# Kernel optimization log

Measured on AMD Instinct MI355X. Metric: run time of the kernel, lower is better.

Reference implementation:

```python
import jax, jax.numpy as jnp
import numpy as np

BATCH = 64
N_NODES = 1000
SEQ = 12
FEAT = 4          # in_features_per_node // N_history
IN_CH = 48        # in_features_per_node, also GAT out_channels
HEADS = 2
OUT_FEAT = 2      # out_features_per_node
H1, H2 = 256, 128
N_TOTAL = BATCH * N_NODES
E = 1024000


def setup_inputs() -> dict:
    key = jax.random.key(0)
    ks = jax.random.split(key, 16)
    s = 0.05
    return {
        "x": jax.random.normal(ks[0], (N_TOTAL, IN_CH), jnp.float32),
        "edge_index": jax.random.randint(ks[1], (2, E), 0, N_TOTAL, jnp.int64),
        "W_gat": jax.random.normal(ks[2], (IN_CH, HEADS * IN_CH), jnp.float32) * s,
        "att_src": jax.random.normal(ks[3], (HEADS, IN_CH), jnp.float32) * s,
        "att_dst": jax.random.normal(ks[4], (HEADS, IN_CH), jnp.float32) * s,
        "gat_bias": jax.random.normal(ks[5], (IN_CH,), jnp.float32) * s,
        "W_ih1": jax.random.normal(ks[6], (4 * H1, N_NODES * FEAT), jnp.float32) * s,
        "W_hh1": jax.random.normal(ks[7], (4 * H1, H1), jnp.float32) * s,
        "b1": jnp.zeros((4 * H1,), jnp.float32),
        "W_ih2": jax.random.normal(ks[8], (4 * H2, H1), jnp.float32) * s,
        "W_hh2": jax.random.normal(ks[9], (4 * H2, H2), jnp.float32) * s,
        "b2": jnp.zeros((4 * H2,), jnp.float32),
        "W_out": jax.random.normal(ks[10], (N_NODES * OUT_FEAT, H2), jnp.float32) * s,
        "b_out": jnp.zeros((N_NODES * OUT_FEAT,), jnp.float32),
    }


def _gat_conv(x, edge_index, W_gat, att_src, att_dst, gat_bias):
    """PyG GATConv, heads=HEADS, concat=False (mean over heads), add_self_loops=True."""
    N = x.shape[0]
    h = (x @ W_gat).reshape(N, HEADS, IN_CH)              # [N,H,C]
    a_src = jnp.einsum('nhc,hc->nh', h, att_src)          # [N,H]
    a_dst = jnp.einsum('nhc,hc->nh', h, att_dst)
    loops = jnp.arange(N, dtype=edge_index.dtype)
    src = jnp.concatenate([edge_index[0], loops])         # [E+N]
    dst = jnp.concatenate([edge_index[1], loops])
    e = jax.nn.leaky_relu(a_src[src] + a_dst[dst], 0.2)   # [E+N,H]
    # segment-softmax over incoming edges of each destination node
    m = jnp.full((N, HEADS), -jnp.inf, e.dtype).at[dst].max(e)
    w = jnp.exp(e - m[dst])
    denom = jax.ops.segment_sum(w, dst, num_segments=N)
    alpha = w / (denom[dst] + 1e-16)                      # [E+N,H]
    msg = h[src] * alpha[:, :, None]                      # [E+N,H,C]
    out = jax.ops.segment_sum(msg, dst, num_segments=N)   # [N,H,C]
    return out.mean(axis=1) + gat_bias                    # [N,C]


def _lstm(x_seq, W_ih, W_hh, b):
    """Single-layer LSTM, PyTorch gate order (i,f,g,o). x_seq: [T,B,D]."""
    Hs = W_hh.shape[1]
    B = x_seq.shape[1]
    xw = jnp.einsum('tbd,gd->tbg', x_seq, W_ih) + b       # precompute input proj

    def step(carry, xt):
        h, c = carry
        g = xt + h @ W_hh.T
        i, f, gg, o = jnp.split(g, 4, axis=-1)
        i, f, o = jax.nn.sigmoid(i), jax.nn.sigmoid(f), jax.nn.sigmoid(o)
        c = f * c + i * jnp.tanh(gg)
        h = o * jnp.tanh(c)
        return (h, c), h

    h0 = jnp.zeros((B, Hs), x_seq.dtype)
    _, ys = jax.lax.scan(step, (h0, h0), xw)
    return ys                                             # [T,B,Hs]


def reference(x, edge_index, W_gat, att_src, att_dst, gat_bias,
              W_ih1, W_hh1, b1, W_ih2, W_hh2, b2, W_out, b_out):
    g = _gat_conv(x, edge_index, W_gat, att_src, att_dst, gat_bias)  # [N_total, 48]
    # (B, N_nodes, SEQ, FEAT) -> movedim(2,0) -> (SEQ, B, N_nodes*FEAT)
    g = g.reshape(BATCH, N_NODES, SEQ, FEAT)
    g = jnp.moveaxis(g, 2, 0).reshape(SEQ, BATCH, N_NODES * FEAT)
    y = _lstm(g, W_ih1, W_hh1, b1)
    y = _lstm(y, W_ih2, W_hh2, b2)
    last = y[-1]                                          # [B, H2]
    out = last @ W_out.T + b_out                          # [B, N_nodes*OUT_FEAT]
    return out.reshape(BATCH * N_NODES, OUT_FEAT)
```

## Files before the change

### kernel.cpp

```cpp
#include <hip/hip_runtime.h>
#include <hip/hip_fp16.h>
#include <math.h>

#define NTOT   64000
#define NNODE  1000
#define NBATCH 64
#define NSEQ   12
#define NE     1024000

typedef _Float16 half8 __attribute__((ext_vector_type(8)));
typedef float f32x4 __attribute__((ext_vector_type(4)));

__device__ __forceinline__ float lrelu(float x){ return x > 0.f ? x : 0.2f*x; }
__device__ __forceinline__ float sigmoidf_(float x){ return 1.f/(1.f+__expf(-x)); }

__global__ void __launch_bounds__(256) k_gat_count(const float* __restrict__ x, const float* __restrict__ Wg,
                       const float* __restrict__ att_s, const float* __restrict__ att_d,
                       __half* __restrict__ hfeat, float* __restrict__ asrc, float* __restrict__ adst,
                       const int* __restrict__ ei, int* __restrict__ cnt){
  if (blockIdx.x >= 250){
    int e = (blockIdx.x - 250)*256 + threadIdx.x;
    if (e < NE) atomicAdd(&cnt[ei[NE + e]], 1);
    return;
  }
  __shared__ __align__(16) float Ws[48*96];
  __shared__ float as_s[96], ad_s[96];
  for (int i = threadIdx.x; i < 48*96; i += 256) Ws[i] = Wg[i];
  if (threadIdx.x < 96){ as_s[threadIdx.x] = att_s[threadIdx.x]; ad_s[threadIdx.x] = att_d[threadIdx.x]; }
  __syncthreads();
  int n = blockIdx.x * 256 + threadIdx.x;
  float xr[48];
  const float4* xv = (const float4*)(x + (size_t)n*48);
  #pragma unroll
  for (int q = 0; q < 12; ++q){ float4 v = xv[q]; xr[q*4]=v.x; xr[q*4+1]=v.y; xr[q*4+2]=v.z; xr[q*4+3]=v.w; }
  float a0=0.f,a1=0.f,d0=0.f,d1=0.f;
  __half* hrow = hfeat + (size_t)n*96;
  float prev = 0.f;
  for (int j = 0; j < 96; ++j){
    float acc = 0.f;
    #pragma unroll
    for (int k = 0; k < 48; ++k) acc += xr[k]*Ws[k*96+j];
    if (j & 1){
      __half2 p; p.x = __float2half(prev); p.y = __float2half(acc);
      *(__half2*)(hrow + j - 1) = p;
    } else prev = acc;
    if (j < 48){ a0 += acc*as_s[j]; d0 += acc*ad_s[j]; }
    else       { a1 += acc*as_s[j]; d1 += acc*ad_s[j]; }
  }
  asrc[n*2]=a0; asrc[n*2+1]=a1; adst[n*2]=d0; adst[n*2+1]=d1;
}

__global__ void __launch_bounds__(256) k_scan1(const int* __restrict__ cnt, int* __restrict__ wsum){
  int w = (blockIdx.x*256 + threadIdx.x) >> 6;
  int lane = threadIdx.x & 63;
  int v = cnt[w*64 + lane];
  int t = v;
  #pragma unroll
  for (int d = 1; d < 64; d <<= 1) t += __shfl_xor(t, d);
  if (lane == 0) wsum[w] = t;
}

__global__ void __launch_bounds__(1024) k_scan2(int* __restrict__ wsum){
  __shared__ int tmp[1024];
  int k = threadIdx.x;
  int v = (k < 1000) ? wsum[k] : 0;
  tmp[k] = v; __syncthreads();
  for (int d = 1; d < 1024; d <<= 1){
    int t = (k >= d) ? tmp[k-d] : 0;
    __syncthreads();
    tmp[k] += t;
    __syncthreads();
  }
  if (k < 1000) wsum[k] = tmp[k] - v;
}

__global__ void __launch_bounds__(256) k_scan3(const int* __restrict__ cnt, const int* __restrict__ wpre,
                                               int* __restrict__ offs, int* __restrict__ cursor){
  int w = (blockIdx.x*256 + threadIdx.x) >> 6;
  int lane = threadIdx.x & 63;
  int i = w*64 + lane;
  int v = cnt[i];
  int x = v;
  #pragma unroll
  for (int d = 1; d < 64; d <<= 1){
    int t = __shfl_up(x, d);
    if (lane >= d) x += t;
  }
  int excl = wpre[w] + x - v;
  offs[i] = excl; cursor[i] = excl;
  if (i == NTOT-1) offs[NTOT] = excl + v;
}

__global__ void k_scatter(const int* __restrict__ ei, int* __restrict__ cursor, int* __restrict__ csr){
  int e = blockIdx.x*256 + threadIdx.x;
  if (e < NE){
    int d = ei[NE + e], s = ei[e];
    int pos = atomicAdd(&cursor[d], 1);
    csr[pos] = s;
  }
}

__global__ void __launch_bounds__(256) k_node(const __half* __restrict__ hf, const float* __restrict__ asrc,
                      const float* __restrict__ adst, const int* __restrict__ offs,
                      const int* __restrict__ csr, const float* __restrict__ bias,
                      _Float16* __restrict__ xseqh){
  __shared__ float gsh[4][96];
  int wv = threadIdx.x >> 6, lane = threadIdx.x & 63;
  int n = blockIdx.x*4 + wv;
  int off = offs[n], deg = offs[n+1] - off;
  const float2* as2 = (const float2*)asrc;
  float2 adn = ((const float2*)adst)[n];
  float2 asn = as2[n];
  float es0 = __expf(lrelu(asn.x + adn.x));
  float es1 = __expf(lrelu(asn.y + adn.y));
  if (lane < 48){
    int cl = lane;
    bool h0 = (lane < 24);
    float wself = h0 ? es0 : es1;
    float ssum = wself;
    float2 acc;
    {
      __half2 r2 = *(const __half2*)(hf + (size_t)n*96 + 2*cl);
      float2 r = __half22float2(r2);
      acc.x = r.x*wself; acc.y = r.y*wself;
    }
    int i = 0;
    for (; i + 4 <= deg; i += 4){
      int ss[4];
      #pragma unroll
      for (int j = 0; j < 4; ++j) ss[j] = csr[off+i+j];
      float2 aa[4];
      #pragma unroll
      for (int j = 0; j < 4; ++j) aa[j] = as2[ss[j]];
      __half2 rr[4];
      #pragma unroll
      for (int j = 0; j < 4; ++j) rr[j] = *(const __half2*)(hf + (size_t)ss[j]*96 + 2*cl);
      #pragma unroll
      for (int j = 0; j < 4; ++j){
        float w0 = __expf(lrelu(aa[j].x + adn.x));
        float w1 = __expf(lrelu(aa[j].y + adn.y));
        float ws = h0 ? w0 : w1;
        float2 r = __half22float2(rr[j]);
        acc.x += r.x*ws; acc.y += r.y*ws;
        ssum += ws;
      }
    }
    for (; i < deg; ++i){
      int s = csr[off+i];
      float2 a = as2[s];
      __half2 r2 = *(const __half2*)(hf + (size_t)s*96 + 2*cl);
      float w0 = __expf(lrelu(a.x + adn.x));
      float w1 = __expf(lrelu(a.y + adn.y));
      float ws = h0 ? w0 : w1;
      float2 r = __half22float2(r2);
      acc.x += r.x*ws; acc.y += r.y*ws;
      ssum += ws;
    }
    float inv = 1.f/(ssum + 1e-16f);
    gsh[wv][2*cl] = acc.x*inv; gsh[wv][2*cl+1] = acc.y*inv;
  }
  __syncthreads();
  if (lane < 48){
    float g = 0.5f*(gsh[wv][lane] + gsh[wv][48+lane]) + bias[lane];
    int b = n / 1000, node = n - b*1000;
    int t = lane >> 2, f = lane & 3;
    xseqh[((size_t)(t*64 + b))*4000 + node*4 + f] = (_Float16)g;
  }
}

__global__ void __launch_bounds__(256) k_prep(const float* __restrict__ Wih1,
                    const float* __restrict__ Whh1, const float* __restrict__ Wih2,
                    const float* __restrict__ Whh2,
                    _Float16* __restrict__ Bh, __half* __restrict__ dst){
  int blk = blockIdx.x;
  if (blk < 4000){
    int i = blk*256 + threadIdx.x;
    float4 v = *(const float4*)(Wih1 + (size_t)i*4);
    union { _Float16 h[4]; uint2 u; } o;
    o.h[0] = (_Float16)v.x; o.h[1] = (_Float16)v.y;
    o.h[2] = (_Float16)v.z; o.h[3] = (_Float16)v.w;
    *(uint2*)(Bh + (size_t)i*4) = o.u;
    return;
  }
  int i = (blk-4000)*256 + threadIdx.x;
  if (i < 262144){ int q = i>>10, r = i&1023; dst[i] = __float2half(Whh1[r*256+q]); return; }
  i -= 262144;
  if (i < 131072){ int q = i>>9, r = i&511; dst[262144+i] = __float2half(Wih2[r*256+q]); return; }
  i -= 131072;
  if (i < 65536){ int q = i>>9, r = i&511; dst[393216+i] = __float2half(Whh2[(size_t)r*128+q]); }
}

__global__ void __launch_bounds__(256) k_gemm1h(const _Float16* __restrict__ A,
                        const _Float16* __restrict__ B, float* __restrict__ part){
  __shared__ _Float16 As[64*40];
  __shared__ _Float16 Bs[64*40];
  int tid = threadIdx.x;
  int w = tid >> 6, l = tid & 63;
  int m0 = blockIdx.x*64, n0 = blockIdx.y*64;
  int k0 = blockIdx.z*800;
  int fr = l & 15, fk = (l >> 4)*8;
  f32x4 acc0 = {0.f,0.f,0.f,0.f}, acc1 = acc0, acc2 = acc0, acc3 = acc0;
  int ra = tid >> 2, ca = (tid & 3)*8;
  const _Float16* Ap = A + (size_t)(m0+ra)*4000 + k0 + ca;
  const _Float16* Bp = B + (size_t)(n0+ra)*4000 + k0 + ca;
  _Float16* Asw = &As[ra*40 + ca];
  _Float16* Bsw = &Bs[ra*40 + ca];
  half8 pa = *(const half8*)Ap;
  half8 pb = *(const half8*)Bp;
  for (int kk = 0; kk < 800; kk += 32){
    *(half8*)Asw = pa;
    *(half8*)Bsw = pb;
    __syncthreads();
    if (kk + 32 < 800){
      pa = *(const half8*)(Ap + kk + 32);
      pb = *(const half8*)(Bp + kk + 32);
    }
    half8 af  = *(const half8*)&As[(w*16 + fr)*40 + fk];
    half8 bf0 = *(const half8*)&Bs[( 0 + fr)*40 + fk];
    half8 bf1 = *(const half8*)&Bs[(16 + fr)*40 + fk];
    half8 bf2 = *(const half8*)&Bs[(32 + fr)*40 + fk];
    half8 bf3 = *(const half8*)&Bs[(48 + fr)*40 + fk];
    acc0 = __builtin_amdgcn_mfma_f32_16x16x32_f16(af, bf0, acc0, 0, 0, 0);
    acc1 = __builtin_amdgcn_mfma_f32_16x16x32_f16(af, bf1, acc1, 0, 0, 0);
    acc2 = __builtin_amdgcn_mfma_f32_16x16x32_f16(af, bf2, acc2, 0, 0, 0);
    acc3 = __builtin_amdgcn_mfma_f32_16x16x32_f16(af, bf3, acc3, 0, 0, 0);
    __syncthreads();
  }
  int mrow = m0 + w*16 + (l >> 4)*4;
  int ncol = n0 + (l & 15);
  #pragma unroll
  for (int r = 0; r < 4; ++r){
    float* cp = part + ((size_t)blockIdx.z*768 + mrow + r)*1024 + ncol;
    cp[0]  = acc0[r];
    cp[16] = acc1[r];
    cp[32] = acc2[r];
    cp[48] = acc3[r];
  }
}

__global__ void k_red5(const float* __restrict__ part, const float* __restrict__ b1,
                       float* __restrict__ xw1){
  int i = blockIdx.x*256 + threadIdx.x;
  int j = i & 1023;
  float v = b1[j];
  #pragma unroll
  for (int s = 0; s < 5; ++s) v += part[(size_t)s*786432 + i];
  xw1[i] = v;
}

__device__ __forceinline__ void mac8(float* acc, uint4 wv, float hq){
  const __half2* hp = (const __half2*)&wv;
  float2 f0 = __half22float2(hp[0]);
  float2 f1 = __half22float2(hp[1]);
  float2 f2 = __half22float2(hp[2]);
  float2 f3 = __half22float2(hp[3]);
  acc[0] += f0.x*hq; acc[1] += f0.y*hq;
  acc[2] += f1.x*hq; acc[3] += f1.y*hq;
  acc[4] += f2.x*hq; acc[5] += f2.y*hq;
  acc[6] += f3.x*hq; acc[7] += f3.y*hq;
}

__global__ void __launch_bounds__(1024) k_lstm(
    const float* __restrict__ xw1, const __half* __restrict__ W1,
    const __half* __restrict__ W2i, const __half* __restrict__ W2h,
    const float* __restrict__ b2, float* __restrict__ h2o){
  __shared__ float h1s[256];
  __shared__ float h2s[128];
  __shared__ __align__(16) float pA[8192];
  __shared__ __align__(16) float pB[8192];
  int t = threadIdx.x;
  int b = blockIdx.x;
  int kk1 = t >> 7, c1c = (t & 127) * 8;
  int kk2 = t >> 6, c2c = (t & 63) * 8;
  int u2 = t - 256;
  float cc1 = 0.f, cc2 = 0.f;
  float b2r[4] = {0.f,0.f,0.f,0.f};
  if (t >= 256 && t < 384){
    #pragma unroll
    for (int gi = 0; gi < 4; ++gi) b2r[gi] = b2[gi*128 + u2];
  }
  if (t < 256) h1s[t] = 0.f;
  if (t < 128) h2s[t] = 0.f;
  __syncthreads();

  for (int k = 0; k <= NSEQ; ++k){
    float xg[4] = {0.f,0.f,0.f,0.f};
    if (k < NSEQ && t < 256){
      const float* xr = xw1 + ((size_t)k*64 + b)*1024 + t;
      #pragma unroll
      for (int gi = 0; gi < 4; ++gi) xg[gi] = xr[gi*256];
    }
    if (k < NSEQ){
      float acc[8] = {0,0,0,0,0,0,0,0};
      const __half* wp = W1 + (size_t)(kk1*32)*1024 + c1c;
      const float* hb = &h1s[kk1*32];
      #pragma unroll 4
      for (int q = 0; q < 32; ++q)
        mac8(acc, *(const uint4*)(wp + (size_t)q*1024), hb[q]);
      float4 w0; w0.x=acc[0]; w0.y=acc[1]; w0.z=acc[2]; w0.w=acc[3];
      float4 w1; w1.x=acc[4]; w1.y=acc[5]; w1.z=acc[6]; w1.w=acc[7];
      *(float4*)&pA[kk1*1024 + c1c]     = w0;
      *(float4*)&pA[kk1*1024 + c1c + 4] = w1;
    }
    if (k >= 1){
      float acch[8] = {0,0,0,0,0,0,0,0};
      const __half* wi = W2i + (size_t)(kk2*16)*512 + c2c;
      const float* hb1 = &h1s[kk2*16];
      #pragma unroll 4
      for (int q = 0; q < 16; ++q)
        mac8(acch, *(const uint4*)(wi + (size_t)q*512), hb1[q]);
      const __half* wh = W2h + (size_t)(kk2*8)*512 + c2c;
      const float* hb2 = &h2s[kk2*8];
      #pragma unroll 4
      for (int q = 0; q < 8; ++q)
        mac8(acch, *(const uint4*)(wh + (size_t)q*512), hb2[q]);
      float4 w0; w0.x=acch[0]; w0.y=acch[1]; w0.z=acch[2]; w0.w=acch[3];
      float4 w1; w1.x=acch[4]; w1.y=acch[5]; w1.z=acch[6]; w1.w=acch[7];
      *(float4*)&pB[kk2*512 + c2c]     = w0;
      *(float4*)&pB[kk2*512 + c2c + 4] = w1;
    }
    __syncthreads();
    if (k < NSEQ && t < 256){
      float g[4];
      #pragma unroll
      for (int gi = 0; gi < 4; ++gi){
        float s = xg[gi];
        #pragma unroll
        for (int kk = 0; kk < 8; ++kk) s += pA[kk*1024 + gi*256 + t];
        g[gi] = s;
      }
      float i_ = sigmoidf_(g[0]);
      float f_ = sigmoidf_(g[1]);
      float gg = tanhf(g[2]);
      float o_ = sigmoidf_(g[3]);
      cc1 = f_*cc1 + i_*gg;
      h1s[t] = o_*tanhf(cc1);
    }
    if (k >= 1 && t >= 256 && t < 384){
      float g[4];
      #pragma unroll
      for (int gi = 0; gi < 4; ++gi){
        float s = b2r[gi];
        #pragma unroll
        for (int kk = 0; kk < 16; ++kk) s += pB[kk*512 + gi*128 + u2];
        g[gi] = s;
      }
      float i_ = sigmoidf_(g[0]);
      float f_ = sigmoidf_(g[1]);
      float gg = tanhf(g[2]);
      float o_ = sigmoidf_(g[3]);
      cc2 = f_*cc2 + i_*gg;
      h2s[u2] = o_*tanhf(cc2);
    }
    __syncthreads();
  }
  if (t >= 256 && t < 384) h2o[(size_t)b*128 + u2] = h2s[u2];
}

__global__ void __launch_bounds__(256) k_out(const float* __restrict__ h2, const float* __restrict__ Wout,
                     const float* __restrict__ bout, float* __restrict__ out){
  __shared__ __align__(16) float hs[8][128];
  int t = threadIdx.x;
  int b0 = blockIdx.y * 8;
  #pragma unroll
  for (int r = 0; r < 4; ++r){
    int idx = r*256 + t;
    hs[idx >> 7][idx & 127] = h2[(size_t)(b0 + (idx >> 7))*128 + (idx & 127)];
  }
  __syncthreads();
  if (t >= 250) return;
  int j = blockIdx.x*250 + t;
  const float4* w = (const float4*)(Wout + (size_t)j*128);
  float bj = bout[j];
  float d[8];
  #pragma unroll
  for (int bb = 0; bb < 8; ++bb) d[bb] = bj;
  for (int q = 0; q < 32; ++q){
    float4 wv = w[q];
    #pragma unroll
    for (int bb = 0; bb < 8; ++bb){
      float4 hv = ((const float4*)hs[bb])[q];
      d[bb] += wv.x*hv.x + wv.y*hv.y + wv.z*hv.z + wv.w*hv.w;
    }
  }
  #pragma unroll
  for (int bb = 0; bb < 8; ++bb)
    out[(size_t)(b0+bb)*2000 + j] = d[bb];
}

extern "C" void kernel_launch(void* const* d_in, const int* in_sizes, int n_in,
                              void* d_out, int out_size, void* d_ws, size_t ws_size,
                              hipStream_t stream){
  const float* x     = (const float*)d_in[0];
  const int*   ei    = (const int*)d_in[1];
  const float* Wg    = (const float*)d_in[2];
  const float* att_s = (const float*)d_in[3];
  const float* att_d = (const float*)d_in[4];
  const float* gb    = (const float*)d_in[5];
  const float* Wih1  = (const float*)d_in[6];
  const float* Whh1  = (const float*)d_in[7];
  const float* b1    = (const float*)d_in[8];
  const float* Wih2  = (const float*)d_in[9];
  const float* Whh2  = (const float*)d_in[10];
  const float* b2    = (const float*)d_in[11];
  const float* Wout  = (const float*)d_in[12];
  const float* bout  = (const float*)d_in[13];
  float* out = (float*)d_out;

  char* w = (char*)d_ws;
  _Float16* xseqh = (_Float16*)w;
  char*  hbase = w + 12288000;
  __half* hfeath = (__half*)hbase;
  _Float16* Bh  = (_Float16*)hbase;
  float* xw1    = (float*)(hbase + 8192000);
  __half* W1h   = (__half*)(hbase + 11337728);
  float* h2o    = (float*)(hbase + 12255232);
  float* part   = (float*)(hbase + 12288000);
  char*  p2 = w + 12288000 + 24576000;
  float* asrc   = (float*)(p2);
  float* adst   = (float*)(p2 + 512000);
  int*   cnt    = (int*)(p2 + 1024000);
  int*   offs   = (int*)(p2 + 1280000);
  int*   cursor = (int*)(p2 + 1536256);
  int*   csr    = (int*)(p2 + 1792256);
  int*   wsum   = csr;

  hipMemsetAsync(cnt, 0, NTOT*sizeof(int), stream);

  k_gat_count<<<4250, 256, 0, stream>>>(x, Wg, att_s, att_d, hfeath, asrc, adst, ei, cnt);
  k_scan1<<<250, 256, 0, stream>>>(cnt, wsum);
  k_scan2<<<1, 1024, 0, stream>>>(wsum);
  k_scan3<<<250, 256, 0, stream>>>(cnt, wsum, offs, cursor);
  k_scatter<<<4000, 256, 0, stream>>>(ei, cursor, csr);
  k_node<<<16000, 256, 0, stream>>>(hfeath, asrc, adst, offs, csr, gb, xseqh);

  k_prep<<<5792, 256, 0, stream>>>(Wih1, Whh1, Wih2, Whh2, Bh, W1h);
  k_gemm1h<<<dim3(12,16,5), 256, 0, stream>>>(xseqh, Bh, part);
  k_red5<<<3072, 256, 0, stream>>>(part, b1, xw1);

  k_lstm<<<NBATCH, 1024, 0, stream>>>(xw1, W1h, W1h + 262144, W1h + 393216, b2, h2o);
  k_out<<<dim3(8,8), 256, 0, stream>>>(h2o, Wout, bout, out);
}
```

Baseline: 365.2 us.

## Fuse split-K reduction into LSTM, vectorize GAT projection, unroll edge loop by 8

Removes the k_red5 kernel and has the LSTM kernel sum the five split-K partials plus bias when it loads each timestep's input projection. This saves a launch and a full write and read of the intermediate buffer. The GAT projection now computes four output columns at a time using float4 shared-memory loads, and the aggregation loop gains an 8-wide unrolled path for more memory-level parallelism. The cost is more global loads inside the serial LSTM loop and higher register pressure in the node kernel.

Result: faster. 354.7 us, median of 3 (-2.9%).

```diff
diff --git a/kernel.cpp b/kernel.cpp
--- a/kernel.cpp
+++ b/kernel.cpp
@@ -24,7 +24,8 @@
     return;
   }
   __shared__ __align__(16) float Ws[48*96];
-  __shared__ float as_s[96], ad_s[96];
+  __shared__ __align__(16) float as_s[96];
+  __shared__ __align__(16) float ad_s[96];
   for (int i = threadIdx.x; i < 48*96; i += 256) Ws[i] = Wg[i];
   if (threadIdx.x < 96){ as_s[threadIdx.x] = att_s[threadIdx.x]; ad_s[threadIdx.x] = att_d[threadIdx.x]; }
   __syncthreads();
@@ -35,17 +36,24 @@
   for (int q = 0; q < 12; ++q){ float4 v = xv[q]; xr[q*4]=v.x; xr[q*4+1]=v.y; xr[q*4+2]=v.z; xr[q*4+3]=v.w; }
   float a0=0.f,a1=0.f,d0=0.f,d1=0.f;
   __half* hrow = hfeat + (size_t)n*96;
-  float prev = 0.f;
-  for (int j = 0; j < 96; ++j){
-    float acc = 0.f;
-    #pragma unroll
-    for (int k = 0; k < 48; ++k) acc += xr[k]*Ws[k*96+j];
-    if (j & 1){
-      __half2 p; p.x = __float2half(prev); p.y = __float2half(acc);
-      *(__half2*)(hrow + j - 1) = p;
-    } else prev = acc;
-    if (j < 48){ a0 += acc*as_s[j]; d0 += acc*ad_s[j]; }
-    else       { a1 += acc*as_s[j]; d1 += acc*ad_s[j]; }
+  for (int j4 = 0; j4 < 96; j4 += 4){
+    float ax=0.f, ay=0.f, az=0.f, aw=0.f;
+    #pragma unroll 8
+    for (int k = 0; k < 48; ++k){
+      float4 wv = *(const float4*)&Ws[k*96 + j4];
+      float xk = xr[k];
+      ax += wv.x*xk; ay += wv.y*xk; az += wv.z*xk; aw += wv.w*xk;
+    }
+    __half2 p0; p0.x = __float2half(ax); p0.y = __float2half(ay);
+    __half2 p1; p1.x = __float2half(az); p1.y = __float2half(aw);
+    *(__half2*)(hrow + j4)     = p0;
+    *(__half2*)(hrow + j4 + 2) = p1;
+    float4 as4 = *(const float4*)&as_s[j4];
+    float4 ad4 = *(const float4*)&ad_s[j4];
+    float sdot = ax*as4.x + ay*as4.y + az*as4.z + aw*as4.w;
+    float ddot = ax*ad4.x + ay*ad4.y + az*ad4.z + aw*ad4.w;
+    if (j4 < 48){ a0 += sdot; d0 += ddot; }
+    else        { a1 += sdot; d1 += ddot; }
   }
   asrc[n*2]=a0; asrc[n*2+1]=a1; adst[n*2]=d0; adst[n*2+1]=d1;
 }
@@ -125,6 +133,26 @@
       acc.x = r.x*wself; acc.y = r.y*wself;
     }
     int i = 0;
+    for (; i + 8 <= deg; i += 8){
+      int ss[8];
+      #pragma unroll
+      for (int j = 0; j < 8; ++j) ss[j] = csr[off+i+j];
+      float2 aa[8];
+      #pragma unroll
+      for (int j = 0; j < 8; ++j) aa[j] = as2[ss[j]];
+      __half2 rr[8];
+      #pragma unroll
+      for (int j = 0; j < 8; ++j) rr[j] = *(const __half2*)(hf + (size_t)ss[j]*96 + 2*cl);
+      #pragma unroll
+      for (int j = 0; j < 8; ++j){
+        float w0 = __expf(lrelu(aa[j].x + adn.x));
+        float w1 = __expf(lrelu(aa[j].y + adn.y));
+        float ws = h0 ? w0 : w1;
+        float2 r = __half22float2(rr[j]);
+        acc.x += r.x*ws; acc.y += r.y*ws;
+        ssum += ws;
+      }
+    }
     for (; i + 4 <= deg; i += 4){
       int ss[4];
       #pragma unroll
@@ -238,16 +266,6 @@
   }
 }
 
-__global__ void k_red5(const float* __restrict__ part, const float* __restrict__ b1,
-                       float* __restrict__ xw1){
-  int i = blockIdx.x*256 + threadIdx.x;
-  int j = i & 1023;
-  float v = b1[j];
-  #pragma unroll
-  for (int s = 0; s < 5; ++s) v += part[(size_t)s*786432 + i];
-  xw1[i] = v;
-}
-
 __device__ __forceinline__ void mac8(float* acc, uint4 wv, float hq){
   const __half2* hp = (const __half2*)&wv;
   float2 f0 = __half22float2(hp[0]);
@@ -261,9 +279,10 @@
 }
 
 __global__ void __launch_bounds__(1024) k_lstm(
-    const float* __restrict__ xw1, const __half* __restrict__ W1,
-    const __half* __restrict__ W2i, const __half* __restrict__ W2h,
-    const float* __restrict__ b2, float* __restrict__ h2o){
+    const float* __restrict__ part, const float* __restrict__ b1,
+    const __half* __restrict__ W1, const __half* __restrict__ W2i,
+    const __half* __restrict__ W2h, const float* __restrict__ b2,
+    float* __restrict__ h2o){
   __shared__ float h1s[256];
   __shared__ float h2s[128];
   __shared__ __align__(16) float pA[8192];
@@ -279,6 +298,11 @@
     #pragma unroll
     for (int gi = 0; gi < 4; ++gi) b2r[gi] = b2[gi*128 + u2];
   }
+  float b1r[4] = {0.f,0.f,0.f,0.f};
+  if (t < 256){
+    #pragma unroll
+    for (int gi = 0; gi < 4; ++gi) b1r[gi] = b1[gi*256 + t];
+  }
   if (t < 256) h1s[t] = 0.f;
   if (t < 128) h2s[t] = 0.f;
   __syncthreads();
@@ -286,9 +310,14 @@
   for (int k = 0; k <= NSEQ; ++k){
     float xg[4] = {0.f,0.f,0.f,0.f};
     if (k < NSEQ && t < 256){
-      const float* xr = xw1 + ((size_t)k*64 + b)*1024 + t;
-      #pragma unroll
-      for (int gi = 0; gi < 4; ++gi) xg[gi] = xr[gi*256];
+      const float* pr = part + ((size_t)k*64 + b)*1024 + t;
+      #pragma unroll
+      for (int gi = 0; gi < 4; ++gi){
+        float s = b1r[gi];
+        #pragma unroll
+        for (int ss = 0; ss < 5; ++ss) s += pr[(size_t)ss*786432 + gi*256];
+        xg[gi] = s;
+      }
     }
     if (k < NSEQ){
       float acc[8] = {0,0,0,0,0,0,0,0};
@@ -412,7 +441,6 @@
   char*  hbase = w + 12288000;
   __half* hfeath = (__half*)hbase;
   _Float16* Bh  = (_Float16*)hbase;
-  float* xw1    = (float*)(hbase + 8192000);
   __half* W1h   = (__half*)(hbase + 11337728);
   float* h2o    = (float*)(hbase + 12255232);
   float* part   = (float*)(hbase + 12288000);
@@ -436,8 +464,7 @@
 
   k_prep<<<5792, 256, 0, stream>>>(Wih1, Whh1, Wih2, Whh2, Bh, W1h);
   k_gemm1h<<<dim3(12,16,5), 256, 0, stream>>>(xseqh, Bh, part);
-  k_red5<<<3072, 256, 0, stream>>>(part, b1, xw1);
-
-  k_lstm<<<NBATCH, 1024, 0, stream>>>(xw1, W1h, W1h + 262144, W1h + 393216, b2, h2o);
+
+  k_lstm<<<NBATCH, 1024, 0, stream>>>(part, b1, W1h, W1h + 262144, W1h + 393216, b2, h2o);
   k_out<<<dim3(8,8), 256, 0, stream>>>(h2o, Wout, bout, out);
 }
```
